# Kernel tuning notes

Hardware: AMD Instinct MI355X
Metric: run time of the kernel (lower is better)

The kernel has to match this reference:

```python
import jax, jax.numpy as jnp
import numpy as np

B, T_IN, F, U = 4096, 256, 32, 64
OUT_STEPS = 24


def _lstm_step(x, h, c, W, R, b):
    # Keras LSTMCell: gates z = x@W + h@R + b, split as [i, f, g, o]
    z = x @ W + h @ R + b  # [B, 4U]
    i, f, g, o = jnp.split(z, 4, axis=-1)
    i = jax.nn.sigmoid(i)
    f = jax.nn.sigmoid(f)
    g = jnp.tanh(g)
    o = jax.nn.sigmoid(o)
    c_new = f * c + i * g
    h_new = o * jnp.tanh(c_new)
    return h_new, c_new


def setup_inputs() -> dict:
    key = jax.random.key(0)
    ks = jax.random.split(key, 9)
    s_in = 1.0 / np.sqrt(F)
    s_hid = 1.0 / np.sqrt(U)
    return {
        "inputs": jax.random.normal(ks[0], (B, T_IN, F), jnp.float32),
        "W1": jax.random.normal(ks[1], (F, 4 * U), jnp.float32) * s_in,
        "U1": jax.random.normal(ks[2], (U, 4 * U), jnp.float32) * s_hid,
        "b1": jnp.zeros((4 * U,), jnp.float32),
        "W2": jax.random.normal(ks[3], (F, 4 * U), jnp.float32) * s_in,
        "U2": jax.random.normal(ks[4], (U, 4 * U), jnp.float32) * s_hid,
        "b2": jnp.zeros((4 * U,), jnp.float32),
        "Wd": jax.random.normal(ks[5], (U, F), jnp.float32) * s_hid,
        "bd": jnp.zeros((F,), jnp.float32),
    }


def reference(inputs, W1, U1, b1, W2, U2, b2, Wd, bd):
    batch = inputs.shape[0]
    units = U1.shape[0]
    h0 = jnp.zeros((batch, units), inputs.dtype)
    c0 = jnp.zeros((batch, units), inputs.dtype)

    # ---- warmup: run lstm_cell_warmup over the input sequence ----
    def warm_step(carry, x_t):
        h, c = carry
        h, c = _lstm_step(x_t, h, c, W1, U1, b1)
        return (h, c), None

    (h, c), _ = jax.lax.scan(warm_step, (h0, c0), jnp.swapaxes(inputs, 0, 1))
    pred0 = h @ Wd + bd  # [B, F]

    def dec_step(carry, _):
        pred, h, c = carry
        h, c = _lstm_step(pred, h, c, W2, U2, b2)
        pred = h @ Wd + bd
        return (pred, h, c), pred

    _, preds_rest = jax.lax.scan(dec_step, (pred0, h, c), None, length=OUT_STEPS - 1)
    preds = jnp.concatenate([pred0[None], preds_rest], axis=0)  # [T_out, B, F]
    return jnp.transpose(preds, (1, 0, 2))  # [B, T_out, F]
```

## Files before the change

### kernel.cpp

```cpp
#include <hip/hip_runtime.h>
#include <math.h>

#define T_STEPS 256
#define Fdim 32
#define Udim 64
#define G4 256
#define OUT_STEPS 24
#define ROWS 16
#define NBLK 256
#define NTHR 512
#define HBS 72
#define CHUNK 16
#define NCHUNK 16
#define LOG2E 1.4426950408889634f

typedef __attribute__((ext_vector_type(8))) short short8;
typedef __attribute__((ext_vector_type(4))) float f32x4;

__device__ __forceinline__ short f2bf(float f) {
    union { float f; unsigned u; } v; v.f = f;
    unsigned r = v.u + 0x7FFFu + ((v.u >> 16) & 1u);
    return (short)(r >> 16);
}
__device__ __forceinline__ float bf2f(short s) {
    union { unsigned u; float f; } v; v.u = ((unsigned)(unsigned short)s) << 16;
    return v.f;
}
__device__ __forceinline__ float frcp(float v) { return __builtin_amdgcn_rcpf(v); }
__device__ __forceinline__ float fexp2(float v) { return __builtin_amdgcn_exp2f(v); }

__device__ __forceinline__ unsigned pkbf(float lo, float hi) {
    unsigned r;
    asm("v_cvt_pk_bf16_f32 %0, %1, %2" : "=v"(r) : "v"(lo), "v"(hi));
    return r;
}

__device__ __forceinline__ float cell_h(const f32x4 a, float& cst) {
    float A  = fexp2(-a[0]);
    float Bv = fexp2(a[2]);
    float rf = frcp(1.0f + fexp2(-a[1]));
    float ig = (Bv - 1.0f) * frcp((1.0f + A) * (1.0f + Bv));
    cst = fmaf(cst, rf, ig);
    float C  = fexp2(-a[3]);
    float D  = fexp2(2.0f * LOG2E * cst);
    return (D - 1.0f) * frcp((1.0f + C) * (1.0f + D));
}

#define BAR() asm volatile("s_waitcnt lgkmcnt(0)\n\ts_barrier" ::: "memory")

#define MFMA __builtin_amdgcn_mfma_f32_16x16x32_bf16

__global__ __launch_bounds__(NTHR, 2)
void lstm_v13(const float* __restrict__ x,
              const float* __restrict__ W1, const float* __restrict__ U1, const float* __restrict__ b1,
              const float* __restrict__ W2, const float* __restrict__ U2, const float* __restrict__ b2,
              const float* __restrict__ Wd, const float* __restrict__ bd,
              float* __restrict__ out)
{
    __shared__ __align__(16) short hb[2][ROWS][HBS];
    __shared__ __align__(16) short xs[CHUNK][ROWS][HBS];
    __shared__ __align__(16) float WdLf[Udim][Fdim];
    __shared__ __align__(16) unsigned short UeffB[Udim][G4];
    __shared__ float beffL[G4];

    const int tid = threadIdx.x;
    const int l   = tid & 63;
    const int w   = tid >> 6;
    const int q   = l >> 4;
    const int m   = l & 15;
    const int brow = blockIdx.x * ROWS;

    const int f4  = tid & 7;
    const int tt  = (tid >> 3) & 15;
    const int xr0 = tid >> 7;
    float4 pf[4];
#pragma unroll
    for (int i = 0; i < 4; ++i)
        pf[i] = *(const float4*)&x[((size_t)(brow + xr0 + 4 * i) * T_STEPS + tt) * Fdim + f4 * 4];

    short8 wa1[2][3];
    f32x4 bs1[2];
#pragma unroll
    for (int nt = 0; nt < 2; ++nt) {
        const int unit_a = w * 8 + (m >> 2) * 2 + nt;
        const int gate_a = m & 3;
        const int col = gate_a * 64 + unit_a;
        const float sA = (gate_a == 2) ? 2.0f * LOG2E : LOG2E;
#pragma unroll
        for (int kt = 0; kt < 3; ++kt) {
            short8 fa;
#pragma unroll
            for (int j = 0; j < 8; ++j) {
                const int k = kt * 32 + q * 8 + j;
                fa[j] = f2bf(((k < Udim) ? U1[k * G4 + col] : W1[(k - Udim) * G4 + col]) * sA);
            }
            wa1[nt][kt] = fa;
        }
        const int unit_d = w * 8 + q * 2 + nt;
#pragma unroll
        for (int g = 0; g < 4; ++g) {
            const float sD = (g == 2) ? 2.0f * LOG2E : LOG2E;
            bs1[nt][g] = b1[g * 64 + unit_d] * sD;
        }
    }

    short8 wdh[2], wdlo[2];
    f32x4 bdC;
    {
        const int wsel = (w < 2) ? w : 0;
#pragma unroll
        for (int kt = 0; kt < 2; ++kt) {
            short8 fh, fl;
#pragma unroll
            for (int j = 0; j < 8; ++j) {
                const float v = Wd[(kt * 32 + q * 8 + j) * Fdim + 16 * wsel + m];
                const short hi = f2bf(v);
                fh[j] = hi;
                fl[j] = f2bf(v - bf2f(hi));
            }
            wdh[kt] = fh;
            wdlo[kt] = fl;
        }
#pragma unroll
        for (int g = 0; g < 4; ++g) bdC[g] = bd[16 * wsel + q * 4 + g];
    }

    const int hw = w * 8 + q * 2;

    for (int idx = tid; idx < 2 * ROWS * HBS; idx += NTHR) ((short*)hb)[idx] = 0;
    for (int idx = tid; idx < Udim * Fdim; idx += NTHR) ((float*)WdLf)[idx] = Wd[idx];
    BAR();
    {
        const int colf = tid & 255;
        const int kh   = tid >> 8;
        float w2col[Fdim];
#pragma unroll
        for (int f = 0; f < Fdim; ++f) w2col[f] = W2[f * G4 + colf];
        const int gatef = colf >> 6;
        const float sAf = (gatef == 2) ? 2.0f * LOG2E : LOG2E;
#pragma unroll
        for (int e = 0; e < 32; ++e) {
            const int k = kh * 32 + e;
            float v = U2[(size_t)k * G4 + colf];
#pragma unroll
            for (int f = 0; f < Fdim; ++f)
                v = fmaf(WdLf[k][f], w2col[f], v);
            UeffB[k][colf] = (unsigned short)f2bf(v * sAf);
        }
        if (tid < G4) {
            float v = b2[colf];
#pragma unroll
            for (int f = 0; f < Fdim; ++f) v = fmaf(bd[f], w2col[f], v);
            beffL[colf] = v;
        }
    }
    BAR();

    short8 wa2[2][2];
    f32x4 bs2[2];
#pragma unroll
    for (int nt = 0; nt < 2; ++nt) {
        const int unit_a = w * 8 + (m >> 2) * 2 + nt;
        const int col = (m & 3) * 64 + unit_a;
#pragma unroll
        for (int kt = 0; kt < 2; ++kt) {
            short8 fb;
#pragma unroll
            for (int j = 0; j < 8; ++j)
                fb[j] = (short)UeffB[kt * 32 + q * 8 + j][col];
            wa2[nt][kt] = fb;
        }
        const int unit_d = w * 8 + q * 2 + nt;
#pragma unroll
        for (int g = 0; g < 4; ++g) {
            const float sD = (g == 2) ? 2.0f * LOG2E : LOG2E;
            bs2[nt][g] = beffL[g * 64 + unit_d] * sD;
        }
    }

    float cst[2] = {0.f, 0.f};

    for (int c = 0; c < NCHUNK; ++c) {
#pragma unroll
        for (int i = 0; i < 4; ++i) {
            uint2 pk;
            pk.x = pkbf(pf[i].x, pf[i].y);
            pk.y = pkbf(pf[i].z, pf[i].w);
            *(uint2*)&xs[tt][xr0 + 4 * i][f4 * 4] = pk;
        }
        if (c + 1 < NCHUNK) {
#pragma unroll
            for (int i = 0; i < 4; ++i)
                pf[i] = *(const float4*)&x[((size_t)(brow + xr0 + 4 * i) * T_STEPS + ((c + 1) * CHUNK + tt)) * Fdim + f4 * 4];
        }
        BAR();

        short8 xf[CHUNK];
#pragma unroll
        for (int t = 0; t < CHUNK; ++t)
            xf[t] = *(const short8*)&xs[t][m][q * 8];

#pragma unroll
        for (int t2 = 0; t2 < CHUNK; ++t2) {
            const int p = t2 & 1;

            const short8 b0  = *(const short8*)&hb[p][m][q * 8];
            const short8 b1v = *(const short8*)&hb[p][m][32 + q * 8];

            f32x4 a0 = MFMA(wa1[0][2], xf[t2], bs1[0], 0, 0, 0);
            f32x4 a1 = MFMA(wa1[1][2], xf[t2], bs1[1], 0, 0, 0);
            a0 = MFMA(wa1[0][0], b0, a0, 0, 0, 0);
            a1 = MFMA(wa1[1][0], b0, a1, 0, 0, 0);
            a0 = MFMA(wa1[0][1], b1v, a0, 0, 0, 0);
            a1 = MFMA(wa1[1][1], b1v, a1, 0, 0, 0);

            const float h0 = cell_h(a0, cst[0]);
            const float h1 = cell_h(a1, cst[1]);
            *(unsigned*)&hb[1 - p][m][hw] = pkbf(h0, h1);
            BAR();
        }
    }

    int dp = 0;
    for (int s = 1; s < OUT_STEPS; ++s) {
        const short8 b0p = *(const short8*)&hb[dp][m][q * 8];
        const short8 b1p = *(const short8*)&hb[dp][m][32 + q * 8];

        f32x4 a0 = MFMA(wa2[0][0], b0p, bs2[0], 0, 0, 0);
        f32x4 a1 = MFMA(wa2[1][0], b0p, bs2[1], 0, 0, 0);
        a0 = MFMA(wa2[0][1], b1p, a0, 0, 0, 0);
        a1 = MFMA(wa2[1][1], b1p, a1, 0, 0, 0);

        const float h0 = cell_h(a0, cst[0]);
        const float h1 = cell_h(a1, cst[1]);
        *(unsigned*)&hb[1 - dp][m][hw] = pkbf(h0, h1);

        if (w < 2) {
            f32x4 pz = MFMA(wdh[0], b0p, bdC, 0, 0, 0);
            pz = MFMA(wdh[1], b1p, pz, 0, 0, 0);
            pz = MFMA(wdlo[0], b0p, pz, 0, 0, 0);
            pz = MFMA(wdlo[1], b1p, pz, 0, 0, 0);
            *(f32x4*)&out[(size_t)(brow + m) * (OUT_STEPS * Fdim) + (s - 1) * Fdim + 16 * w + q * 4] = pz;
        }
        BAR();
        dp = 1 - dp;
    }
    if (w < 2) {
        const short8 b0p = *(const short8*)&hb[dp][m][q * 8];
        const short8 b1p = *(const short8*)&hb[dp][m][32 + q * 8];
        f32x4 pz = MFMA(wdh[0], b0p, bdC, 0, 0, 0);
        pz = MFMA(wdh[1], b1p, pz, 0, 0, 0);
        pz = MFMA(wdlo[0], b0p, pz, 0, 0, 0);
        pz = MFMA(wdlo[1], b1p, pz, 0, 0, 0);
        *(f32x4*)&out[(size_t)(brow + m) * (OUT_STEPS * Fdim) + (OUT_STEPS - 1) * Fdim + 16 * w + q * 4] = pz;
    }
}

extern "C" void kernel_launch(void* const* d_in, const int* in_sizes, int n_in,
                              void* d_out, int out_size, void* d_ws, size_t ws_size,
                              hipStream_t stream) {
    (void)in_sizes; (void)n_in; (void)out_size; (void)d_ws; (void)ws_size;
    const float* x  = (const float*)d_in[0];
    const float* W1 = (const float*)d_in[1];
    const float* U1 = (const float*)d_in[2];
    const float* b1 = (const float*)d_in[3];
    const float* W2 = (const float*)d_in[4];
    const float* U2 = (const float*)d_in[5];
    const float* b2 = (const float*)d_in[6];
    const float* Wd = (const float*)d_in[7];
    const float* bd = (const float*)d_in[8];
    float* out = (float*)d_out;

    lstm_v13<<<dim3(NBLK), dim3(NTHR), 0, stream>>>(
        x, W1, U1, b1, W2, U2, b2, Wd, bd, out);
}
```

Before: 279.2 us.

## Pack two independent 16-row batch groups into each 1024-thread block

Each block now holds two groups of 8 waves, and each group runs its own 16-row LSTM recurrence with separate h and x buffers in LDS. The block count halves to 128 and the thread count doubles to 1024. The one-time Ueff precompute and the x chunk staging are shared across both groups, so their cost is spread over twice the rows. In exchange, each per-step barrier now syncs 16 waves, and the launch-bounds occupancy hint is dropped, which may lower occupancy or increase register pressure.

```diff
diff --git a/kernel.cpp b/kernel.cpp
--- a/kernel.cpp
+++ b/kernel.cpp
@@ -7,8 +7,9 @@
 #define G4 256
 #define OUT_STEPS 24
 #define ROWS 16
-#define NBLK 256
-#define NTHR 512
+#define GROUPS 2
+#define NBLK 128
+#define NTHR 1024
 #define HBS 72
 #define CHUNK 16
 #define NCHUNK 16
@@ -50,15 +51,15 @@
 
 #define MFMA __builtin_amdgcn_mfma_f32_16x16x32_bf16
 
-__global__ __launch_bounds__(NTHR, 2)
-void lstm_v13(const float* __restrict__ x,
+__global__ __launch_bounds__(NTHR)
+void lstm_v14(const float* __restrict__ x,
               const float* __restrict__ W1, const float* __restrict__ U1, const float* __restrict__ b1,
               const float* __restrict__ W2, const float* __restrict__ U2, const float* __restrict__ b2,
               const float* __restrict__ Wd, const float* __restrict__ bd,
               float* __restrict__ out)
 {
-    __shared__ __align__(16) short hb[2][ROWS][HBS];
-    __shared__ __align__(16) short xs[CHUNK][ROWS][HBS];
+    __shared__ __align__(16) short hb[GROUPS][2][ROWS][HBS];
+    __shared__ __align__(16) short xs[GROUPS][CHUNK][ROWS][HBS];
     __shared__ __align__(16) float WdLf[Udim][Fdim];
     __shared__ __align__(16) unsigned short UeffB[Udim][G4];
     __shared__ float beffL[G4];
@@ -66,23 +67,26 @@
     const int tid = threadIdx.x;
     const int l   = tid & 63;
     const int w   = tid >> 6;
+    const int g   = w >> 3;
+    const int w8  = w & 7;
     const int q   = l >> 4;
     const int m   = l & 15;
-    const int brow = blockIdx.x * ROWS;
-
-    const int f4  = tid & 7;
-    const int tt  = (tid >> 3) & 15;
-    const int xr0 = tid >> 7;
+    const int brow_blk = blockIdx.x * (GROUPS * ROWS);
+    const int brow_g   = brow_blk + g * ROWS;
+
+    const int f4 = tid & 7;
+    const int tt = (tid >> 3) & 15;
+    const int xr = tid >> 7;
     float4 pf[4];
 #pragma unroll
     for (int i = 0; i < 4; ++i)
-        pf[i] = *(const float4*)&x[((size_t)(brow + xr0 + 4 * i) * T_STEPS + tt) * Fdim + f4 * 4];
+        pf[i] = *(const float4*)&x[((size_t)(brow_blk + xr + 8 * i) * T_STEPS + tt) * Fdim + f4 * 4];
 
     short8 wa1[2][3];
     f32x4 bs1[2];
 #pragma unroll
     for (int nt = 0; nt < 2; ++nt) {
-        const int unit_a = w * 8 + (m >> 2) * 2 + nt;
+        const int unit_a = w8 * 8 + (m >> 2) * 2 + nt;
         const int gate_a = m & 3;
         const int col = gate_a * 64 + unit_a;
         const float sA = (gate_a == 2) ? 2.0f * LOG2E : LOG2E;
@@ -96,18 +100,18 @@
             }
             wa1[nt][kt] = fa;
         }
-        const int unit_d = w * 8 + q * 2 + nt;
-#pragma unroll
-        for (int g = 0; g < 4; ++g) {
-            const float sD = (g == 2) ? 2.0f * LOG2E : LOG2E;
-            bs1[nt][g] = b1[g * 64 + unit_d] * sD;
+        const int unit_d = w8 * 8 + q * 2 + nt;
+#pragma unroll
+        for (int g2 = 0; g2 < 4; ++g2) {
+            const float sD = (g2 == 2) ? 2.0f * LOG2E : LOG2E;
+            bs1[nt][g2] = b1[g2 * 64 + unit_d] * sD;
         }
     }
 
     short8 wdh[2], wdlo[2];
     f32x4 bdC;
     {
-        const int wsel = (w < 2) ? w : 0;
+        const int wsel = (w8 < 2) ? w8 : 0;
 #pragma unroll
         for (int kt = 0; kt < 2; ++kt) {
             short8 fh, fl;
@@ -122,25 +126,24 @@
             wdlo[kt] = fl;
         }
 #pragma unroll
-        for (int g = 0; g < 4; ++g) bdC[g] = bd[16 * wsel + q * 4 + g];
-    }
-
-    const int hw = w * 8 + q * 2;
-
-    for (int idx = tid; idx < 2 * ROWS * HBS; idx += NTHR) ((short*)hb)[idx] = 0;
+        for (int g2 = 0; g2 < 4; ++g2) bdC[g2] = bd[16 * wsel + q * 4 + g2];
+    }
+
+    const int hw = w8 * 8 + q * 2;
+
+    for (int idx = tid; idx < GROUPS * 2 * ROWS * HBS; idx += NTHR) ((short*)hb)[idx] = 0;
     for (int idx = tid; idx < Udim * Fdim; idx += NTHR) ((float*)WdLf)[idx] = Wd[idx];
     BAR();
     {
         const int colf = tid & 255;
-        const int kh   = tid >> 8;
+        const int kq   = tid >> 8;
         float w2col[Fdim];
 #pragma unroll
         for (int f = 0; f < Fdim; ++f) w2col[f] = W2[f * G4 + colf];
-        const int gatef = colf >> 6;
-        const float sAf = (gatef == 2) ? 2.0f * LOG2E : LOG2E;
-#pragma unroll
-        for (int e = 0; e < 32; ++e) {
-            const int k = kh * 32 + e;
+        const float sAf = ((colf >> 6) == 2) ? 2.0f * LOG2E : LOG2E;
+#pragma unroll
+        for (int e = 0; e < 16; ++e) {
+            const int k = kq * 16 + e;
             float v = U2[(size_t)k * G4 + colf];
 #pragma unroll
             for (int f = 0; f < Fdim; ++f)
@@ -160,7 +163,7 @@
     f32x4 bs2[2];
 #pragma unroll
     for (int nt = 0; nt < 2; ++nt) {
-        const int unit_a = w * 8 + (m >> 2) * 2 + nt;
+        const int unit_a = w8 * 8 + (m >> 2) * 2 + nt;
         const int col = (m & 3) * 64 + unit_a;
 #pragma unroll
         for (int kt = 0; kt < 2; ++kt) {
@@ -170,11 +173,11 @@
                 fb[j] = (short)UeffB[kt * 32 + q * 8 + j][col];
             wa2[nt][kt] = fb;
         }
-        const int unit_d = w * 8 + q * 2 + nt;
-#pragma unroll
-        for (int g = 0; g < 4; ++g) {
-            const float sD = (g == 2) ? 2.0f * LOG2E : LOG2E;
-            bs2[nt][g] = beffL[g * 64 + unit_d] * sD;
+        const int unit_d = w8 * 8 + q * 2 + nt;
+#pragma unroll
+        for (int g2 = 0; g2 < 4; ++g2) {
+            const float sD = (g2 == 2) ? 2.0f * LOG2E : LOG2E;
+            bs2[nt][g2] = beffL[g2 * 64 + unit_d] * sD;
         }
     }
 
@@ -183,48 +186,52 @@
     for (int c = 0; c < NCHUNK; ++c) {
 #pragma unroll
         for (int i = 0; i < 4; ++i) {
+            const int r = xr + 8 * i;
             uint2 pk;
             pk.x = pkbf(pf[i].x, pf[i].y);
             pk.y = pkbf(pf[i].z, pf[i].w);
-            *(uint2*)&xs[tt][xr0 + 4 * i][f4 * 4] = pk;
+            *(uint2*)&xs[r >> 4][tt][r & 15][f4 * 4] = pk;
         }
         if (c + 1 < NCHUNK) {
 #pragma unroll
             for (int i = 0; i < 4; ++i)
-                pf[i] = *(const float4*)&x[((size_t)(brow + xr0 + 4 * i) * T_STEPS + ((c + 1) * CHUNK + tt)) * Fdim + f4 * 4];
+                pf[i] = *(const float4*)&x[((size_t)(brow_blk + xr + 8 * i) * T_STEPS + ((c + 1) * CHUNK + tt)) * Fdim + f4 * 4];
         }
         BAR();
 
-        short8 xf[CHUNK];
-#pragma unroll
-        for (int t = 0; t < CHUNK; ++t)
-            xf[t] = *(const short8*)&xs[t][m][q * 8];
-
-#pragma unroll
-        for (int t2 = 0; t2 < CHUNK; ++t2) {
-            const int p = t2 & 1;
-
-            const short8 b0  = *(const short8*)&hb[p][m][q * 8];
-            const short8 b1v = *(const short8*)&hb[p][m][32 + q * 8];
-
-            f32x4 a0 = MFMA(wa1[0][2], xf[t2], bs1[0], 0, 0, 0);
-            f32x4 a1 = MFMA(wa1[1][2], xf[t2], bs1[1], 0, 0, 0);
-            a0 = MFMA(wa1[0][0], b0, a0, 0, 0, 0);
-            a1 = MFMA(wa1[1][0], b0, a1, 0, 0, 0);
-            a0 = MFMA(wa1[0][1], b1v, a0, 0, 0, 0);
-            a1 = MFMA(wa1[1][1], b1v, a1, 0, 0, 0);
-
-            const float h0 = cell_h(a0, cst[0]);
-            const float h1 = cell_h(a1, cst[1]);
-            *(unsigned*)&hb[1 - p][m][hw] = pkbf(h0, h1);
-            BAR();
+#pragma unroll
+        for (int half = 0; half < 2; ++half) {
+            short8 xf[8];
+#pragma unroll
+            for (int t = 0; t < 8; ++t)
+                xf[t] = *(const short8*)&xs[g][half * 8 + t][m][q * 8];
+
+#pragma unroll
+            for (int t2 = 0; t2 < 8; ++t2) {
+                const int p = t2 & 1;
+
+                const short8 b0  = *(const short8*)&hb[g][p][m][q * 8];
+                const short8 b1v = *(const short8*)&hb[g][p][m][32 + q * 8];
+
+                f32x4 a0 = MFMA(wa1[0][2], xf[t2], bs1[0], 0, 0, 0);
+                f32x4 a1 = MFMA(wa1[1][2], xf[t2], bs1[1], 0, 0, 0);
+                a0 = MFMA(wa1[0][0], b0, a0, 0, 0, 0);
+                a1 = MFMA(wa1[1][0], b0, a1, 0, 0, 0);
+                a0 = MFMA(wa1[0][1], b1v, a0, 0, 0, 0);
+                a1 = MFMA(wa1[1][1], b1v, a1, 0, 0, 0);
+
+                const float h0 = cell_h(a0, cst[0]);
+                const float h1 = cell_h(a1, cst[1]);
+                *(unsigned*)&hb[g][1 - p][m][hw] = pkbf(h0, h1);
+                BAR();
+            }
         }
     }
 
     int dp = 0;
     for (int s = 1; s < OUT_STEPS; ++s) {
-        const short8 b0p = *(const short8*)&hb[dp][m][q * 8];
-        const short8 b1p = *(const short8*)&hb[dp][m][32 + q * 8];
+        const short8 b0p = *(const short8*)&hb[g][dp][m][q * 8];
+        const short8 b1p = *(const short8*)&hb[g][dp][m][32 + q * 8];
 
         f32x4 a0 = MFMA(wa2[0][0], b0p, bs2[0], 0, 0, 0);
         f32x4 a1 = MFMA(wa2[1][0], b0p, bs2[1], 0, 0, 0);
@@ -233,26 +240,26 @@
 
         const float h0 = cell_h(a0, cst[0]);
         const float h1 = cell_h(a1, cst[1]);
-        *(unsigned*)&hb[1 - dp][m][hw] = pkbf(h0, h1);
-
-        if (w < 2) {
+        *(unsigned*)&hb[g][1 - dp][m][hw] = pkbf(h0, h1);
+
+        if (w8 < 2) {
             f32x4 pz = MFMA(wdh[0], b0p, bdC, 0, 0, 0);
             pz = MFMA(wdh[1], b1p, pz, 0, 0, 0);
             pz = MFMA(wdlo[0], b0p, pz, 0, 0, 0);
             pz = MFMA(wdlo[1], b1p, pz, 0, 0, 0);
-            *(f32x4*)&out[(size_t)(brow + m) * (OUT_STEPS * Fdim) + (s - 1) * Fdim + 16 * w + q * 4] = pz;
+            *(f32x4*)&out[(size_t)(brow_g + m) * (OUT_STEPS * Fdim) + (s - 1) * Fdim + 16 * w8 + q * 4] = pz;
         }
         BAR();
         dp = 1 - dp;
     }
-    if (w < 2) {
-        const short8 b0p = *(const short8*)&hb[dp][m][q * 8];
-        const short8 b1p = *(const short8*)&hb[dp][m][32 + q * 8];
+    if (w8 < 2) {
+        const short8 b0p = *(const short8*)&hb[g][dp][m][q * 8];
+        const short8 b1p = *(const short8*)&hb[g][dp][m][32 + q * 8];
         f32x4 pz = MFMA(wdh[0], b0p, bdC, 0, 0, 0);
         pz = MFMA(wdh[1], b1p, pz, 0, 0, 0);
         pz = MFMA(wdlo[0], b0p, pz, 0, 0, 0);
         pz = MFMA(wdlo[1], b1p, pz, 0, 0, 0);
-        *(f32x4*)&out[(size_t)(brow + m) * (OUT_STEPS * Fdim) + (OUT_STEPS - 1) * Fdim + 16 * w + q * 4] = pz;
+        *(f32x4*)&out[(size_t)(brow_g + m) * (OUT_STEPS * Fdim) + (OUT_STEPS - 1) * Fdim + 16 * w8 + q * 4] = pz;
     }
 }
 
@@ -271,6 +278,6 @@
     const float* bd = (const float*)d_in[8];
     float* out = (float*)d_out;
 
-    lstm_v13<<<dim3(NBLK), dim3(NTHR), 0, stream>>>(
+    lstm_v14<<<dim3(NBLK), dim3(NTHR), 0, stream>>>(
         x, W1, U1, b1, W2, U2, b2, Wd, bd, out);
 }
```

Result: slower. 365.8 us (+31.0%).
